# Performance work log

Measured on AMD Instinct MI355X. Metric: run time of the kernel, lower is better.

## Reference

```python
import jax, jax.numpy as jnp
import numpy as np

B, N, D = 16, 8192, 384   # examples, sentences per example, embedding dim
KN = 16                   # neighbors per node (kNN degree)
K, H, STEPS = 8, 128, 3   # coin dim, hidden dim, walk steps


def setup_inputs() -> dict:
    key = jax.random.key(0)
    ks = jax.random.split(key, 12)
    s = 0.02
    return {
        "sent_embs": jax.random.normal(ks[0], (B, N, D), dtype=jnp.float32),
        "q_embs": jax.random.normal(ks[1], (B, D), dtype=jnp.float32),
        "neighbors": jax.random.randint(ks[2], (B, N, KN), 0, N, dtype=jnp.int32),
        # coin_net: Linear(2D->H), ReLU, Linear(H->K)
        "coin_w1": jax.random.normal(ks[3], (2 * D, H), dtype=jnp.float32) * s,
        "coin_b1": jnp.zeros((H,), dtype=jnp.float32),
        "coin_w2": jax.random.normal(ks[4], (H, K), dtype=jnp.float32) * s,
        "coin_b2": jnp.zeros((K,), dtype=jnp.float32),
        # path_net: Linear(D+K+D->H), ReLU, Linear(H->1)
        "path_w1": jax.random.normal(ks[5], (D + K + D, H), dtype=jnp.float32) * s,
        "path_b1": jnp.zeros((H,), dtype=jnp.float32),
        "path_w2": jax.random.normal(ks[6], (H, 1), dtype=jnp.float32) * s,
        "path_b2": jnp.zeros((1,), dtype=jnp.float32),
    }


def _mlp(x, w1, b1, w2, b2):
    return jax.nn.relu(x @ w1 + b1) @ w2 + b2


def _forward(sent_embs, q_embs, neighbors,
             coin_w1, coin_b1, coin_w2, coin_b2,
             path_w1, path_b1, path_w2, path_b2):
    b, n, d = sent_embs.shape
    k = coin_w2.shape[1]
    q_bcast = jnp.broadcast_to(q_embs[:, None, :], (b, n, d))

    # coin amplitudes per node: [B, N, K]
    amps = _mlp(jnp.concatenate([sent_embs, q_bcast], axis=-1),
                coin_w1, coin_b1, coin_w2, coin_b2)

    # initial uniform walk state: 1/sqrt(N*K)
    state = jnp.full((b, n, k), 1.0 / np.sqrt(n * k), dtype=sent_embs.dtype)

    # adjacency = self-loop + edges row -> neighbors[row]; A @ X == X + masked neighbor gather-sum
    valid = (neighbors >= 0) & (neighbors < n)           # [B, N, KN]
    safe_nbrs = jnp.where(valid, neighbors, 0)
    batch_idx = jnp.arange(b)[:, None, None]

    for _ in range(STEPS):
        ns = state * amps                                # coin step
        gathered = ns[batch_idx, safe_nbrs]              # [B, N, KN, K]
        gathered = jnp.where(valid[..., None], gathered, 0.0)
        ns = ns + gathered.sum(axis=2)                   # sparse.mm(A, ns)
        norm = jnp.linalg.norm(ns.reshape(b, -1), axis=1)[:, None, None]
        state = ns / jnp.where(norm > 0, norm, 1.0)      # renormalize (guard norm==0)

    path_in = jnp.concatenate([sent_embs, state, q_bcast], axis=-1)  # [B, N, D+K+D]
    logits = _mlp(path_in, path_w1, path_b1, path_w2, path_b2)[..., 0]  # [B, N]
    return logits


def reference(sent_embs, q_embs, neighbors,
              coin_w1, coin_b1, coin_w2, coin_b2,
              path_w1, path_b1, path_w2, path_b2):
    return _forward(sent_embs, q_embs, neighbors,
                    coin_w1, coin_b1, coin_w2, coin_b2,
                    path_w1, path_b1, path_w2, path_b2)
```

## Files before the change

### kernel.cpp

```cpp
#include <hip/hip_runtime.h>

#define B_SZ 16
#define N_SZ 8192
#define D_SZ 384
#define KN_SZ 16
#define K_SZ 8
#define H_SZ 128
#define M_TOTAL (B_SZ * N_SZ)
#define KSTEPS 12
#define MT64 (M_TOTAL / 64)
#define CK 128
#define LDSB_STRIDE 144
#define HS_STRIDE 130

typedef short short8 __attribute__((ext_vector_type(8)));
typedef short short4v __attribute__((ext_vector_type(4)));
typedef float floatx4 __attribute__((ext_vector_type(4)));

__device__ __forceinline__ unsigned short f2bf(float f) {
    unsigned u = __builtin_bit_cast(unsigned, f);
    u += 0x7FFFu + ((u >> 16) & 1u);
    return (unsigned short)(u >> 16);
}
__device__ __forceinline__ float bf2f(unsigned short b) {
    unsigned u = ((unsigned)b) << 16;
    return __builtin_bit_cast(float, u);
}
__device__ __forceinline__ unsigned pkbf(float a, float b) {
    unsigned r;
    asm("v_cvt_pk_bf16_f32 %0, %1, %2" : "=v"(r) : "v"(a), "v"(b));
    return r;
}

__global__ void prep_kernel(const float* __restrict__ q_embs,
                            const float* __restrict__ coin_w1,
                            const float* __restrict__ coin_b1,
                            const float* __restrict__ path_w1,
                            const float* __restrict__ path_b1,
                            unsigned short* __restrict__ wswz,
                            float* __restrict__ qcoin, float* __restrict__ qpath,
                            float* __restrict__ norms) {
    int blk = blockIdx.x;
    int t = threadIdx.x;
    if (blk < 384) {
        int f = blk * 256 + t;
        int j  = f & 7;
        int l  = (f >> 3) & 63;
        int ss = (f >> 9) % KSTEPS;
        int ct = f / (KSTEPS * 512);
        int k = ss * 32 + ((l >> 4) << 3) + j;
        int n = ct * 16 + (l & 15);
        float v = (n < H_SZ) ? coin_w1[k * H_SZ + n]
                             : path_w1[k * H_SZ + (n - H_SZ)];
        wswz[f] = f2bf(v);
    } else if (blk == 384) {
        if (t < B_SZ) norms[t] = 0.f;
    } else {
        int b = blk - 385;
        const float* q = q_embs + b * D_SZ;
        if (t < H_SZ) {
            float acc = coin_b1[t];
            for (int d = 0; d < D_SZ; d++)
                acc += q[d] * coin_w1[(D_SZ + d) * H_SZ + t];
            qcoin[b * H_SZ + t] = acc;
        } else if (t < 2 * H_SZ) {
            int h = t - H_SZ;
            float acc = path_b1[h];
            for (int d = 0; d < D_SZ; d++)
                acc += q[d] * path_w1[(D_SZ + K_SZ + d) * H_SZ + h];
            qpath[b * H_SZ + h] = acc;
        }
    }
}

__global__ __launch_bounds__(256)
void gemm_fused(const float* __restrict__ sent,
                const unsigned short* __restrict__ wswz,
                const float* __restrict__ qcoin,
                const float* __restrict__ coin_w2,
                const float* __restrict__ coin_b2,
                unsigned short* __restrict__ hpathB,
                float* __restrict__ amps) {
    __shared__ __align__(16) short als[2 * 64 * LDSB_STRIDE];
    __shared__ float w2s[H_SZ * K_SZ];
    short* buf0 = als;
    short* buf1 = als + 64 * LDSB_STRIDE;
    const int tid = threadIdx.x;
    const int wave = tid >> 6, lane = tid & 63;
    const int m_lane = lane & 15, quad = lane >> 4;
    const int mt = blockIdx.x;
    const int b = mt >> 7;
    const float* abase = sent + (size_t)mt * 64 * D_SZ;
    const int row8 = tid >> 5;
    const int c4   = tid & 31;

    for (int i = tid; i < H_SZ * K_SZ; i += 256) w2s[i] = coin_w2[i];

    const unsigned short* wbase = wswz + (size_t)wave * 4 * KSTEPS * 512 + lane * 8;
    floatx4 acc[4][4];
#pragma unroll
    for (int rt = 0; rt < 4; rt++)
#pragma unroll
        for (int c = 0; c < 4; c++) acc[rt][c] = (floatx4){0.f, 0.f, 0.f, 0.f};

    float4 v[8];

#define STAGE_LOAD(CHUNK)                                                        \
    _Pragma("unroll")                                                            \
    for (int u = 0; u < 8; u++)                                                  \
        v[u] = *(const float4*)(abase + (size_t)(row8 + u * 8) * D_SZ +          \
                                (CHUNK) * CK + c4 * 4);

#define STAGE_STORE(BUF)                                                         \
    _Pragma("unroll")                                                            \
    for (int u = 0; u < 8; u++) {                                                \
        int2 p;                                                                  \
        p.x = (int)pkbf(v[u].x, v[u].y);                                         \
        p.y = (int)pkbf(v[u].z, v[u].w);                                         \
        *(int2*)&(BUF)[(row8 + u * 8) * LDSB_STRIDE + c4 * 4] = p;               \
    }

#define MMA_CHUNK(BUF, CHUNK)                                                    \
    _Pragma("unroll")                                                            \
    for (int sl = 0; sl < 4; sl++) {                                             \
        const int s = (CHUNK) * 4 + sl;                                          \
        short8 bfr[4];                                                           \
        _Pragma("unroll")                                                        \
        for (int cc = 0; cc < 4; cc++)                                           \
            bfr[cc] = *(const short8*)(wbase + (size_t)(cc * KSTEPS + s) * 512); \
        short8 af[4];                                                            \
        _Pragma("unroll")                                                        \
        for (int rt = 0; rt < 4; rt++)                                           \
            af[rt] = *(const short8*)&(BUF)[(rt * 16 + m_lane) * LDSB_STRIDE +   \
                                            sl * 32 + quad * 8];                 \
        _Pragma("unroll")                                                        \
        for (int rt = 0; rt < 4; rt++)                                           \
            _Pragma("unroll")                                                    \
            for (int cc = 0; cc < 4; cc++)                                       \
                acc[rt][cc] = __builtin_amdgcn_mfma_f32_16x16x32_bf16(           \
                    af[rt], bfr[cc], acc[rt][cc], 0, 0, 0);                      \
    }

    STAGE_LOAD(0);
    STAGE_STORE(buf0);
    __syncthreads();
    STAGE_LOAD(1);
    MMA_CHUNK(buf0, 0);
    STAGE_STORE(buf1);
    __syncthreads();
    STAGE_LOAD(2);
    MMA_CHUNK(buf1, 1);
    STAGE_STORE(buf0);
    __syncthreads();
    MMA_CHUNK(buf0, 2);

    if (wave >= 2) {
        const int colw = (wave & 1) * 64;
#pragma unroll
        for (int rt = 0; rt < 4; rt++) {
            int mt16 = mt * 4 + rt;
#pragma unroll
            for (int c = 0; c < 4; c++) {
                int col = colw + c * 16 + m_lane;
                int2 p;
                p.x = (int)pkbf(acc[rt][c][0], acc[rt][c][1]);
                p.y = (int)pkbf(acc[rt][c][2], acc[rt][c][3]);
                *(int2*)(hpathB + (size_t)mt16 * 2048 + col * 16 + quad * 4) = p;
            }
        }
    }
    __syncthreads();

    float* hs = (float*)als;
    if (wave < 2) {
        const int colw = wave * 64;
        float qc[4];
#pragma unroll
        for (int c = 0; c < 4; c++)
            qc[c] = qcoin[b * H_SZ + colw + c * 16 + m_lane];
#pragma unroll
        for (int rt = 0; rt < 4; rt++)
#pragma unroll
            for (int c = 0; c < 4; c++) {
                int colj = colw + c * 16 + m_lane;
#pragma unroll
                for (int j = 0; j < 4; j++) {
                    int row = rt * 16 + quad * 4 + j;
                    float hv = acc[rt][c][j] + qc[c];
                    hs[row * HS_STRIDE + colj] = hv > 0.f ? hv : 0.f;
                }
            }
    }
    __syncthreads();

    {
        const int r = tid >> 2;
        const int kk = (tid & 3) * 2;
        float a0 = coin_b2[kk], a1 = coin_b2[kk + 1];
#pragma unroll 8
        for (int c = 0; c < H_SZ; c++) {
            float hv = hs[r * HS_STRIDE + c];
            float2 w = *(const float2*)&w2s[c * 8 + kk];
            a0 += hv * w.x; a1 += hv * w.y;
        }
        const size_t m = (size_t)mt * 64 + r;
        *(float2*)(amps + m * 8 + kk) = make_float2(a0, a1);
    }
#undef STAGE_LOAD
#undef STAGE_STORE
#undef MMA_CHUNK
}

__global__ __launch_bounds__(256)
void walk_step(const float* __restrict__ z,
               const int* __restrict__ neighbors,
               const float* __restrict__ amps,
               float* __restrict__ outz,
               float* __restrict__ norms, int last, float presc) {
    const int g = blockIdx.x * 256 + threadIdx.x;
    const int m = g >> 1, half = g & 1;
    const int b = m >> 13;
    const size_t nbase = (size_t)b << 13;
    const int off = half * 4;

    float4 v = *(const float4*)(z + (size_t)m * 8 + off);
    int nbr[KN_SZ];
    const int4* nb4 = (const int4*)(neighbors + (size_t)m * KN_SZ);
#pragma unroll
    for (int i = 0; i < 4; i++) *(int4*)&nbr[i * 4] = nb4[i];
#pragma unroll
    for (int i = 0; i < KN_SZ; i++) {
        int nn = nbr[i];
        if (nn >= 0 && nn < N_SZ) {
            float4 gv = *(const float4*)(z + (nbase + nn) * 8 + off);
            v.x += gv.x; v.y += gv.y; v.z += gv.z; v.w += gv.w;
        }
    }
    v.x *= presc; v.y *= presc; v.z *= presc; v.w *= presc;
    if (!last) {
        float4 a = *(const float4*)(amps + (size_t)m * 8 + off);
        v.x *= a.x; v.y *= a.y; v.z *= a.z; v.w *= a.w;
        *(float4*)(outz + (size_t)m * 8 + off) = v;
    } else {
        *(float4*)(outz + (size_t)m * 8 + off) = v;
        float ss = v.x * v.x + v.y * v.y + v.z * v.z + v.w * v.w;
#pragma unroll
        for (int o = 32; o > 0; o >>= 1) ss += __shfl_down(ss, o);
        __shared__ float blocksum;
        if (threadIdx.x == 0) blocksum = 0.f;
        __syncthreads();
        if ((threadIdx.x & 63) == 0) atomicAdd(&blocksum, ss);
        __syncthreads();
        if (threadIdx.x == 0) atomicAdd(&norms[b], blocksum);
    }
}

__global__ __launch_bounds__(256)
void logits_kernel(const unsigned short* __restrict__ hpathB,
                   const float* __restrict__ qpath,
                   const float* __restrict__ u2,
                   const float* __restrict__ norms,
                   const float* __restrict__ path_w1,
                   const float* __restrict__ path_w2,
                   const float* __restrict__ path_b2,
                   float* __restrict__ out) {
    __shared__ float w1t[4 * 260];
    __shared__ float w2sp[4 * 33];
    __shared__ float qps[4 * 33];
    const int tid = threadIdx.x;
    const int mbase = blockIdx.x * 64;
    const int b = mbase >> 13;
    for (int i2 = tid; i2 < H_SZ * K_SZ; i2 += 256) {
        int h = i2 >> 3, j = i2 & 7;
        w1t[(h >> 5) * 260 + (h & 31) * 8 + j] = path_w1[(D_SZ + j) * H_SZ + h];
    }
    if (tid < H_SZ) {
        int idx = (tid >> 5) * 33 + (tid & 31);
        w2sp[idx] = path_w2[tid];
        qps[idx]  = qpath[b * H_SZ + tid];
    }
    __syncthreads();

    const int m = mbase + (tid >> 2);
    const int seg = tid & 3;
    float ssq = norms[b];
    float inv = ssq > 0.f ? rsqrtf(ssq) : 1.0f;
    float st[K_SZ];
    {
        float4 s0 = *(const float4*)(u2 + (size_t)m * 8);
        float4 s1 = *(const float4*)(u2 + (size_t)m * 8 + 4);
        st[0] = s0.x * inv; st[1] = s0.y * inv; st[2] = s0.z * inv; st[3] = s0.w * inv;
        st[4] = s1.x * inv; st[5] = s1.y * inv; st[6] = s1.z * inv; st[7] = s1.w * inv;
    }
    const unsigned short* hb = hpathB + (size_t)(m >> 4) * 2048 + (m & 15);
    const float* w1b = &w1t[seg * 260];
    const float* w2b = &w2sp[seg * 33];
    const float* qpb = &qps[seg * 33];
    const int hseg = seg * 32;

    float acc = 0.f;
#pragma unroll 8
    for (int i = 0; i < 32; i++) {
        float hv = bf2f(hb[(hseg + i) * 16]) + qpb[i];
        float4 wa = *(const float4*)&w1b[i * 8];
        float4 wb = *(const float4*)&w1b[i * 8 + 4];
        hv += st[0]*wa.x + st[1]*wa.y + st[2]*wa.z + st[3]*wa.w
            + st[4]*wb.x + st[5]*wb.y + st[6]*wb.z + st[7]*wb.w;
        hv = hv > 0.f ? hv : 0.f;
        acc += hv * w2b[i];
    }
    acc += __shfl_xor(acc, 1);
    acc += __shfl_xor(acc, 2);
    if (seg == 0) out[m] = acc + path_b2[0];
}

extern "C" void kernel_launch(void* const* d_in, const int* in_sizes, int n_in,
                              void* d_out, int out_size, void* d_ws, size_t ws_size,
                              hipStream_t stream) {
    const float* sent      = (const float*)d_in[0];
    const float* q_embs    = (const float*)d_in[1];
    const int*   neighbors = (const int*)d_in[2];
    const float* coin_w1   = (const float*)d_in[3];
    const float* coin_b1   = (const float*)d_in[4];
    const float* coin_w2   = (const float*)d_in[5];
    const float* coin_b2   = (const float*)d_in[6];
    const float* path_w1   = (const float*)d_in[7];
    const float* path_b1   = (const float*)d_in[8];
    const float* path_w2   = (const float*)d_in[9];
    const float* path_b2   = (const float*)d_in[10];
    float* out = (float*)d_out;

    char* ws = (char*)d_ws;
    unsigned short* wswz = (unsigned short*)ws;
    float* qcoin = (float*)(ws + 196608);
    float* qpath = (float*)(ws + 204800);
    float* norms = (float*)(ws + 212992);
    unsigned short* hpathB = (unsigned short*)(ws + 213248);
    float* amps = (float*)(ws + 33767680);
    float* zA   = (float*)(ws + 37961984);
    float* zB   = (float*)(ws + 42156288);

    prep_kernel<<<401, 256, 0, stream>>>(q_embs, coin_w1, coin_b1, path_w1, path_b1,
                                         wswz, qcoin, qpath, norms);
    gemm_fused<<<MT64, 256, 0, stream>>>(sent, wswz, qcoin, coin_w2, coin_b2,
                                         hpathB, amps);
    walk_step<<<2 * M_TOTAL / 256, 256, 0, stream>>>(amps, neighbors, amps, zB, norms, 0, 1.0f / 256.0f);
    walk_step<<<2 * M_TOTAL / 256, 256, 0, stream>>>(zB, neighbors, amps, zA, norms, 0, 1.0f);
    walk_step<<<2 * M_TOTAL / 256, 256, 0, stream>>>(zA, neighbors, amps, zB, norms, 1, 1.0f);
    logits_kernel<<<M_TOTAL / 64, 256, 0, stream>>>(hpathB, qpath, zB, norms,
                                                    path_w1, path_w2, path_b2, out);
}
```

Measured before the change: 402.9 us.

## Fuse three walk steps into one LDS-resident kernel per batch and channel

Replaces the three separate walk-step launches with one kernel where each block owns one batch and one coin channel, keeping the full node state in shared memory and double-buffering across steps. Neighbor gathers then hit LDS instead of global memory and the intermediate state round-trips disappear. In exchange, only 128 large blocks are launched, and the neighbor index array is re-read by every channel block for every step, multiplying index traffic.

Measured after the change: 393.8 us. -2.3%, faster.

```diff
diff --git a/kernel.cpp b/kernel.cpp
--- a/kernel.cpp
+++ b/kernel.cpp
@@ -211,47 +211,65 @@
 #undef MMA_CHUNK
 }
 
-__global__ __launch_bounds__(256)
-void walk_step(const float* __restrict__ z,
-               const int* __restrict__ neighbors,
-               const float* __restrict__ amps,
-               float* __restrict__ outz,
-               float* __restrict__ norms, int last, float presc) {
-    const int g = blockIdx.x * 256 + threadIdx.x;
-    const int m = g >> 1, half = g & 1;
-    const int b = m >> 13;
-    const size_t nbase = (size_t)b << 13;
-    const int off = half * 4;
-
-    float4 v = *(const float4*)(z + (size_t)m * 8 + off);
-    int nbr[KN_SZ];
-    const int4* nb4 = (const int4*)(neighbors + (size_t)m * KN_SZ);
-#pragma unroll
-    for (int i = 0; i < 4; i++) *(int4*)&nbr[i * 4] = nb4[i];
-#pragma unroll
-    for (int i = 0; i < KN_SZ; i++) {
-        int nn = nbr[i];
-        if (nn >= 0 && nn < N_SZ) {
-            float4 gv = *(const float4*)(z + (nbase + nn) * 8 + off);
-            v.x += gv.x; v.y += gv.y; v.z += gv.z; v.w += gv.w;
+__global__ __launch_bounds__(1024)
+void walk_fused(const float* __restrict__ amps,
+                const int* __restrict__ neighbors,
+                float* __restrict__ zfinal,
+                float* __restrict__ norms) {
+    __shared__ float z0buf[N_SZ];
+    __shared__ float z1buf[N_SZ];
+    __shared__ float bsum;
+    const int tid = threadIdx.x;
+    const int b = blockIdx.x >> 3;
+    const int k = blockIdx.x & 7;
+    const size_t nodebase = (size_t)b * N_SZ;
+
+    float a[8];
+#pragma unroll
+    for (int u = 0; u < 8; u++) {
+        int n = u * 1024 + tid;
+        a[u] = amps[(nodebase + n) * 8 + k];
+        z0buf[n] = a[u] * (1.0f / 256.0f);
+    }
+    if (tid == 0) bsum = 0.f;
+    __syncthreads();
+
+    float* zc = z0buf;
+    float* zn = z1buf;
+    float ss = 0.f;
+#pragma unroll
+    for (int step = 0; step < 3; step++) {
+#pragma unroll
+        for (int u = 0; u < 8; u++) {
+            const int n = u * 1024 + tid;
+            const int4* nb4 = (const int4*)(neighbors + (nodebase + n) * KN_SZ);
+            int4 q0 = nb4[0], q1 = nb4[1], q2 = nb4[2], q3 = nb4[3];
+            float v = zc[n];
+            int idx[16] = {q0.x, q0.y, q0.z, q0.w, q1.x, q1.y, q1.z, q1.w,
+                           q2.x, q2.y, q2.z, q2.w, q3.x, q3.y, q3.z, q3.w};
+#pragma unroll
+            for (int i = 0; i < 16; i++) {
+                int nn = idx[i];
+                if ((unsigned)nn < (unsigned)N_SZ) v += zc[nn];
+            }
+            if (step < 2) v *= a[u];
+            zn[n] = v;
+            if (step == 2) ss += v * v;
         }
-    }
-    v.x *= presc; v.y *= presc; v.z *= presc; v.w *= presc;
-    if (!last) {
-        float4 a = *(const float4*)(amps + (size_t)m * 8 + off);
-        v.x *= a.x; v.y *= a.y; v.z *= a.z; v.w *= a.w;
-        *(float4*)(outz + (size_t)m * 8 + off) = v;
-    } else {
-        *(float4*)(outz + (size_t)m * 8 + off) = v;
-        float ss = v.x * v.x + v.y * v.y + v.z * v.z + v.w * v.w;
-#pragma unroll
-        for (int o = 32; o > 0; o >>= 1) ss += __shfl_down(ss, o);
-        __shared__ float blocksum;
-        if (threadIdx.x == 0) blocksum = 0.f;
         __syncthreads();
-        if ((threadIdx.x & 63) == 0) atomicAdd(&blocksum, ss);
-        __syncthreads();
-        if (threadIdx.x == 0) atomicAdd(&norms[b], blocksum);
+        float* t = zc; zc = zn; zn = t;
+    }
+
+#pragma unroll
+    for (int o = 32; o > 0; o >>= 1) ss += __shfl_down(ss, o);
+    if ((tid & 63) == 0) atomicAdd(&bsum, ss);
+    __syncthreads();
+    if (tid == 0) atomicAdd(&norms[b], bsum);
+
+#pragma unroll
+    for (int u = 0; u < 8; u++) {
+        int n = u * 1024 + tid;
+        zfinal[(nodebase + n) * 8 + k] = zc[n];
     }
 }
 
@@ -337,16 +355,13 @@
     float* norms = (float*)(ws + 212992);
     unsigned short* hpathB = (unsigned short*)(ws + 213248);
     float* amps = (float*)(ws + 33767680);
-    float* zA   = (float*)(ws + 37961984);
-    float* zB   = (float*)(ws + 42156288);
+    float* zB   = (float*)(ws + 37961984);
 
     prep_kernel<<<401, 256, 0, stream>>>(q_embs, coin_w1, coin_b1, path_w1, path_b1,
                                          wswz, qcoin, qpath, norms);
     gemm_fused<<<MT64, 256, 0, stream>>>(sent, wswz, qcoin, coin_w2, coin_b2,
                                          hpathB, amps);
-    walk_step<<<2 * M_TOTAL / 256, 256, 0, stream>>>(amps, neighbors, amps, zB, norms, 0, 1.0f / 256.0f);
-    walk_step<<<2 * M_TOTAL / 256, 256, 0, stream>>>(zB, neighbors, amps, zA, norms, 0, 1.0f);
-    walk_step<<<2 * M_TOTAL / 256, 256, 0, stream>>>(zA, neighbors, amps, zB, norms, 1, 1.0f);
+    walk_fused<<<B_SZ * K_SZ, 1024, 0, stream>>>(amps, neighbors, zB, norms);
     logits_kernel<<<M_TOTAL / 64, 256, 0, stream>>>(hpathB, qpath, zB, norms,
                                                     path_w1, path_w2, path_b2, out);
 }
```
